# Optimization experiments

Hardware: AMD Instinct MI355X
Metric: run time of the kernel (lower is better)

## Reference

```python
import jax, jax.numpy as jnp
import numpy as np

B, T, D, H, DH, F, E, TOPK = 4, 1024, 1024, 16, 64, 4096, 8, 2
GATE_TEMP = 0.9
EPS = 1e-5


def _ln(x, g, b):
    m = jnp.mean(x, axis=-1, keepdims=True)
    v = jnp.mean((x - m) ** 2, axis=-1, keepdims=True)
    return (x - m) * jax.lax.rsqrt(v + EPS) * g + b


def setup_inputs() -> dict:
    key = jax.random.key(0)
    ks = jax.random.split(key, 16)
    s = 0.02
    inp = {
        'x': jax.random.normal(ks[0], (B, T, D), jnp.float32),
        'mask': jnp.tril(jnp.ones((1, 1, T, T), jnp.int32)),  # causal
        'ln1_g': jnp.ones((D,), jnp.float32), 'ln1_b': jnp.zeros((D,), jnp.float32),
        'wq': jax.random.normal(ks[1], (D, D), jnp.float32) * s, 'bq': jnp.zeros((D,), jnp.float32),
        'wk': jax.random.normal(ks[2], (D, D), jnp.float32) * s, 'bk': jnp.zeros((D,), jnp.float32),
        'wv': jax.random.normal(ks[3], (D, D), jnp.float32) * s, 'bv': jnp.zeros((D,), jnp.float32),
        'wo': jax.random.normal(ks[4], (D, D), jnp.float32) * s, 'bo': jnp.zeros((D,), jnp.float32),
        'ln2_g': jnp.ones((D,), jnp.float32), 'ln2_b': jnp.zeros((D,), jnp.float32),
        'gate_w': jax.random.normal(ks[5], (D, E), jnp.float32) * s, 'gate_b': jnp.zeros((E,), jnp.float32),
        'we1': jax.random.normal(ks[6], (E, D, F), jnp.float32) * s, 'be1': jnp.zeros((E, F), jnp.float32),
        'we2': jax.random.normal(ks[7], (E, F, D), jnp.float32) * s, 'be2': jnp.zeros((E, D), jnp.float32),
        'pn_g': jnp.ones((D,), jnp.float32), 'pn_b': jnp.zeros((D,), jnp.float32),
    }
    return inp


def reference(x, mask, ln1_g, ln1_b, wq, bq, wk, bk, wv, bv, wo, bo,
              ln2_g, ln2_b, gate_w, gate_b, we1, be1, we2, be2, pn_g, pn_b):
    # ---- attention branch (dropout = identity in eval) ----
    h = _ln(x, ln1_g, ln1_b)
    q = (h @ wq + bq).reshape(B, T, H, DH).transpose(0, 2, 1, 3)  # [B,H,T,DH]
    k = (h @ wk + bk).reshape(B, T, H, DH).transpose(0, 2, 1, 3)
    v = (h @ wv + bv).reshape(B, T, H, DH).transpose(0, 2, 1, 3)
    att = jnp.einsum('bhtd,bhsd->bhts', q, k) / jnp.sqrt(jnp.float32(DH))
    att = jnp.where(mask == 0, jnp.float32(-1e9), att)
    att = jax.nn.softmax(att, axis=-1)
    out = jnp.einsum('bhts,bhsd->bhtd', att, v).transpose(0, 2, 1, 3).reshape(B, T, D)
    x = x + (out @ wo + bo)

    # ---- MoE branch ----
    h = _ln(x, ln2_g, ln2_b)
    gate_logits = (h @ gate_w + gate_b) / GATE_TEMP        # [B,T,E]
    topk_vals, topk_idx = jax.lax.top_k(gate_logits, TOPK)
    keep = jnp.sum(jax.nn.one_hot(topk_idx, E, dtype=bool), axis=-2)  # [B,T,E] bool
    masked = jnp.where(keep, gate_logits, -jnp.inf)
    gate_probs = jax.nn.softmax(masked, axis=-1)            # [B,T,E]
    # dense all-expert FFN (exact GELU, dropout=identity)
    hid = jax.nn.gelu(jnp.einsum('btd,edf->btef', h, we1) + be1, approximate=False)
    expert_out = jnp.einsum('btef,efd->bted', hid, we2) + be2  # [B,T,E,D]
    moe = jnp.sum(gate_probs[..., None] * expert_out, axis=2)
    moe = _ln(moe, pn_g, pn_b)
    return x + moe
```

## Files before the change

### kernel.cpp

```cpp
#include <hip/hip_runtime.h>
#include <hip/hip_bf16.h>
#include <math.h>

#define B_ 4
#define T_ 1024
#define D_ 1024
#define H_ 16
#define DH_ 64
#define F_ 4096
#define E_ 8
#define NTOK 4096
#define EPS_ 1e-5f

typedef float f32x4 __attribute__((ext_vector_type(4)));
typedef __bf16 bf16x8 __attribute__((ext_vector_type(8)));
typedef _Float16 f16x8 __attribute__((ext_vector_type(8)));

__device__ __forceinline__ unsigned short f2bf(float f) {
    unsigned u = __float_as_uint(f);
    u = u + 0x7fffu + ((u >> 16) & 1u);
    return (unsigned short)(u >> 16);
}

__device__ __forceinline__ void splitf(float x, unsigned short& h, unsigned short& l) {
    _Float16 hf = (_Float16)x;
    _Float16 lf = (_Float16)((x - (float)hf) * 2048.0f);
    h = __builtin_bit_cast(unsigned short, hf);
    l = __builtin_bit_cast(unsigned short, lf);
}

__device__ __forceinline__ void blockreduce2(float& s, float& sq) {
    #pragma unroll
    for (int o = 32; o > 0; o >>= 1) { s += __shfl_xor(s, o); sq += __shfl_xor(sq, o); }
    __shared__ float ls[4], lq[4];
    int w = threadIdx.x >> 6;
    if ((threadIdx.x & 63) == 0) { ls[w] = s; lq[w] = sq; }
    __syncthreads();
    s = ls[0] + ls[1] + ls[2] + ls[3];
    sq = lq[0] + lq[1] + lq[2] + lq[3];
}

__global__ void k_zero(int* __restrict__ cnt) {
    if (threadIdx.x < E_) cnt[threadIdx.x] = 0;
}

__global__ void k_tconv(const float* __restrict__ in, unsigned short* __restrict__ out,
                        int R, int C) {
    __shared__ float tile[32][33];
    int e = blockIdx.z;
    const float* ine = in + (size_t)e * R * C;
    unsigned short* oute = out + (size_t)e * R * C;
    int tx = threadIdx.x & 31, ty = threadIdx.x >> 5;
    int c0 = blockIdx.x * 32, r0 = blockIdx.y * 32;
    #pragma unroll
    for (int j = 0; j < 32; j += 8)
        tile[ty + j][tx] = ine[(size_t)(r0 + ty + j) * C + c0 + tx];
    __syncthreads();
    #pragma unroll
    for (int j = 0; j < 32; j += 8)
        oute[(size_t)(c0 + ty + j) * R + r0 + tx] = f2bf(tile[tx][ty + j]);
}

__global__ void k_tconv_split(const float* __restrict__ w0, const float* __restrict__ w1,
        const float* __restrict__ w2, const float* __restrict__ w3,
        unsigned short* __restrict__ ohi, unsigned short* __restrict__ olo) {
    __shared__ float tile[32][33];
    int z = blockIdx.z;
    const float* in = (z == 0) ? w0 : ((z == 1) ? w1 : ((z == 2) ? w2 : w3));
    unsigned short* oh = ohi + (size_t)z * D_ * D_;
    unsigned short* ol = olo + (size_t)z * D_ * D_;
    int tx = threadIdx.x & 31, ty = threadIdx.x >> 5;
    int c0 = blockIdx.x * 32, r0 = blockIdx.y * 32;
    #pragma unroll
    for (int j = 0; j < 32; j += 8)
        tile[ty + j][tx] = in[(size_t)(r0 + ty + j) * D_ + c0 + tx];
    __syncthreads();
    #pragma unroll
    for (int j = 0; j < 32; j += 8) {
        unsigned short h, l;
        splitf(tile[tx][ty + j], h, l);
        size_t o = (size_t)(c0 + ty + j) * D_ + r0 + tx;
        oh[o] = h; ol[o] = l;
    }
}

__global__ void k_ln1(const float* __restrict__ x, const float* __restrict__ g,
                      const float* __restrict__ b, unsigned short* __restrict__ hh,
                      unsigned short* __restrict__ hl) {
    int row = blockIdx.x, t = threadIdx.x;
    f32x4 v = *(const f32x4*)(x + (size_t)row * D_ + t * 4);
    float s = v.x + v.y + v.z + v.w;
    float sq = v.x * v.x + v.y * v.y + v.z * v.z + v.w * v.w;
    blockreduce2(s, sq);
    float mean = s * (1.0f / D_);
    float var = sq * (1.0f / D_) - mean * mean;
    float inv = rsqrtf(var + EPS_);
    f32x4 gv = *(const f32x4*)(g + t * 4);
    f32x4 bv = *(const f32x4*)(b + t * 4);
    ushort4 oh, ol;
    float o0 = (v.x - mean) * inv * gv.x + bv.x;
    float o1 = (v.y - mean) * inv * gv.y + bv.y;
    float o2 = (v.z - mean) * inv * gv.z + bv.z;
    float o3 = (v.w - mean) * inv * gv.w + bv.w;
    splitf(o0, oh.x, ol.x); splitf(o1, oh.y, ol.y);
    splitf(o2, oh.z, ol.z); splitf(o3, oh.w, ol.w);
    *(ushort4*)(hh + (size_t)row * D_ + t * 4) = oh;
    *(ushort4*)(hl + (size_t)row * D_ + t * 4) = ol;
}

#define LDK2 40
__device__ __forceinline__ void mfma_split(const unsigned short* __restrict__ Ah,
        const unsigned short* __restrict__ Al, int strideA, int m0,
        const unsigned short* __restrict__ Bh, const unsigned short* __restrict__ Bl,
        int strideB, int n0, int K, f32x4 acc1[4][4], f32x4 acc2[4][4]) {
    __shared__ unsigned short AsH[128 * LDK2];
    __shared__ unsigned short AsL[128 * LDK2];
    __shared__ unsigned short BsH[128 * LDK2];
    __shared__ unsigned short BsL[128 * LDK2];
    int t = threadIdx.x;
    int lane = t & 63, w = t >> 6;
    int wm = (w >> 1) * 64, wn = (w & 1) * 64;
    int r = t >> 1, kc = (t & 1) * 16;
    const unsigned short* pAh = Ah + (size_t)(m0 + r) * strideA + kc;
    const unsigned short* pAl = Al + (size_t)(m0 + r) * strideA + kc;
    const unsigned short* pBh = Bh + (size_t)(n0 + r) * strideB + kc;
    const unsigned short* pBl = Bl + (size_t)(n0 + r) * strideB + kc;
    int c15 = lane & 15, fk = (lane >> 4) * 8;
    unsigned short* wAh = &AsH[r * LDK2 + kc];
    unsigned short* wAl = &AsL[r * LDK2 + kc];
    unsigned short* wBh = &BsH[r * LDK2 + kc];
    unsigned short* wBl = &BsL[r * LDK2 + kc];
    uint4 ah0 = *(const uint4*)(pAh);
    uint4 ah1 = *(const uint4*)(pAh + 8);
    uint4 al0 = *(const uint4*)(pAl);
    uint4 al1 = *(const uint4*)(pAl + 8);
    uint4 bh0 = *(const uint4*)(pBh);
    uint4 bh1 = *(const uint4*)(pBh + 8);
    uint4 bl0 = *(const uint4*)(pBl);
    uint4 bl1 = *(const uint4*)(pBl + 8);
    for (int k0 = 0; k0 < K; k0 += 32) {
        __syncthreads();
        *(uint4*)(wAh) = ah0; *(uint4*)(wAh + 8) = ah1;
        *(uint4*)(wAl) = al0; *(uint4*)(wAl + 8) = al1;
        *(uint4*)(wBh) = bh0; *(uint4*)(wBh + 8) = bh1;
        *(uint4*)(wBl) = bl0; *(uint4*)(wBl + 8) = bl1;
        __syncthreads();
        if (k0 + 32 < K) {
            ah0 = *(const uint4*)(pAh + k0 + 32);
            ah1 = *(const uint4*)(pAh + k0 + 40);
            al0 = *(const uint4*)(pAl + k0 + 32);
            al1 = *(const uint4*)(pAl + k0 + 40);
            bh0 = *(const uint4*)(pBh + k0 + 32);
            bh1 = *(const uint4*)(pBh + k0 + 40);
            bl0 = *(const uint4*)(pBl + k0 + 32);
            bl1 = *(const uint4*)(pBl + k0 + 40);
        }
        f16x8 bfh[4], bfl[4];
        #pragma unroll
        for (int i = 0; i < 4; i++) {
            bfh[i] = *(const f16x8*)(&BsH[(wn + c15 + i * 16) * LDK2 + fk]);
            bfl[i] = *(const f16x8*)(&BsL[(wn + c15 + i * 16) * LDK2 + fk]);
        }
        #pragma unroll
        for (int mi = 0; mi < 4; mi++) {
            f16x8 afh = *(const f16x8*)(&AsH[(wm + c15 + mi * 16) * LDK2 + fk]);
            f16x8 afl = *(const f16x8*)(&AsL[(wm + c15 + mi * 16) * LDK2 + fk]);
            #pragma unroll
            for (int ni = 0; ni < 4; ni++) {
                acc1[mi][ni] = __builtin_amdgcn_mfma_f32_16x16x32_f16(afh, bfh[ni], acc1[mi][ni], 0, 0, 0);
                acc2[mi][ni] = __builtin_amdgcn_mfma_f32_16x16x32_f16(afh, bfl[ni], acc2[mi][ni], 0, 0, 0);
                acc2[mi][ni] = __builtin_amdgcn_mfma_f32_16x16x32_f16(afl, bfh[ni], acc2[mi][ni], 0, 0, 0);
            }
        }
    }
}

__global__ __launch_bounds__(256, 2) void k_qkv_split(
        const unsigned short* __restrict__ h1h, const unsigned short* __restrict__ h1l,
        const unsigned short* __restrict__ wth, const unsigned short* __restrict__ wtl,
        const float* __restrict__ bq, const float* __restrict__ bk, const float* __restrict__ bv,
        unsigned short* __restrict__ Qh, unsigned short* __restrict__ Ql,
        unsigned short* __restrict__ Kh, unsigned short* __restrict__ Kl,
        unsigned short* __restrict__ Vh, unsigned short* __restrict__ Vl) {
    int which = blockIdx.z;
    const unsigned short* Bh = wth + (size_t)which * D_ * D_;
    const unsigned short* Bl = wtl + (size_t)which * D_ * D_;
    const float* bias = (which == 0) ? bq : ((which == 1) ? bk : bv);
    unsigned short* Oh = (which == 0) ? Qh : ((which == 1) ? Kh : Vh);
    unsigned short* Ol = (which == 0) ? Ql : ((which == 1) ? Kl : Vl);
    f32x4 a1[4][4], a2[4][4];
    #pragma unroll
    for (int i = 0; i < 4; i++)
        #pragma unroll
        for (int j = 0; j < 4; j++) {
            a1[i][j].x = 0.f; a1[i][j].y = 0.f; a1[i][j].z = 0.f; a1[i][j].w = 0.f;
            a2[i][j].x = 0.f; a2[i][j].y = 0.f; a2[i][j].z = 0.f; a2[i][j].w = 0.f;
        }
    int m0 = blockIdx.y * 128, n0 = blockIdx.x * 128;
    mfma_split(h1h, h1l, D_, m0, Bh, Bl, D_, n0, D_, a1, a2);
    int lane = threadIdx.x & 63, w = threadIdx.x >> 6;
    int wm = (w >> 1) * 64, wn = (w & 1) * 64;
    int c15 = lane & 15, quad = lane >> 4;
    #pragma unroll
    for (int mi = 0; mi < 4; mi++) {
        #pragma unroll
        for (int rr = 0; rr < 4; rr++) {
            int row = m0 + wm + mi * 16 + quad * 4 + rr;
            int bidx = row >> 10, tt = row & 1023;
            #pragma unroll
            for (int ni = 0; ni < 4; ni++) {
                int col = n0 + wn + ni * 16 + c15;
                float vv = a1[mi][ni][rr] + a2[mi][ni][rr] * (1.0f / 2048.0f) + bias[col];
                unsigned short hs, ls;
                splitf(vv, hs, ls);
                size_t idx = (((size_t)bidx * H_ + (col >> 6)) * T_ + tt) * DH_ + (col & 63);
                Oh[idx] = hs; Ol[idx] = ls;
            }
        }
    }
}

__global__ __launch_bounds__(256, 2) void k_proj_split(
        const unsigned short* __restrict__ ah, const unsigned short* __restrict__ al,
        const unsigned short* __restrict__ wh, const unsigned short* __restrict__ wl,
        float* __restrict__ xp) {
    int ks = blockIdx.z;
    f32x4 a1[4][4], a2[4][4];
    #pragma unroll
    for (int i = 0; i < 4; i++)
        #pragma unroll
        for (int j = 0; j < 4; j++) {
            a1[i][j].x = 0.f; a1[i][j].y = 0.f; a1[i][j].z = 0.f; a1[i][j].w = 0.f;
            a2[i][j].x = 0.f; a2[i][j].y = 0.f; a2[i][j].z = 0.f; a2[i][j].w = 0.f;
        }
    int m0 = blockIdx.y * 128, n0 = blockIdx.x * 128;
    mfma_split(ah + ks * 512, al + ks * 512, D_, m0,
               wh + ks * 512, wl + ks * 512, D_, n0, 512, a1, a2);
    float* dst = xp + (size_t)ks * NTOK * D_;
    int lane = threadIdx.x & 63, w = threadIdx.x >> 6;
    int wm = (w >> 1) * 64, wn = (w & 1) * 64;
    int c15 = lane & 15, quad = lane >> 4;
    #pragma unroll
    for (int mi = 0; mi < 4; mi++) {
        #pragma unroll
        for (int rr = 0; rr < 4; rr++) {
            int row = m0 + wm + mi * 16 + quad * 4 + rr;
            #pragma unroll
            for (int ni = 0; ni < 4; ni++) {
                int col = n0 + wn + ni * 16 + c15;
                dst[(size_t)row * D_ + col] = a1[mi][ni][rr] + a2[mi][ni][rr] * (1.0f / 2048.0f);
            }
        }
    }
}

#define NSLOT 40
__device__ __forceinline__ int slot_base(int qt) {
    const int base[16] = {0,1,2,3,4,6,8,10,12,15,18,21,24,28,32,36};
    return base[qt];
}
__device__ __forceinline__ int swzb(int r, int cb) {
    return r * 128 + (cb ^ ((r & 7) << 4));
}
__global__ __launch_bounds__(256, 2) void k_attn1(
        const unsigned short* __restrict__ Qh, const unsigned short* __restrict__ Ql,
        const unsigned short* __restrict__ Kh, const unsigned short* __restrict__ Kl,
        const unsigned short* __restrict__ Vh, const unsigned short* __restrict__ Vl,
        float* __restrict__ opart, float* __restrict__ mlpart) {
    __shared__ unsigned short QsH[64 * 64], QsL[64 * 64];
    __shared__ unsigned short KsH[64 * 64], KsL[64 * 64];
    __shared__ unsigned short VtH[64 * 64], VtL[64 * 64];
    __shared__ unsigned short PsH[64 * 64], PsL[64 * 64];
    int sp = blockIdx.x, qt = blockIdx.y, bh = blockIdx.z;
    int lim = (qt + 1) * 64;
    int s0 = sp * 256;
    if (s0 >= lim) return;
    int ntile = min(4, (lim - s0) >> 6);
    int t = threadIdx.x;
    int lane = t & 63, w = t >> 6;
    int c15 = lane & 15, quad = lane >> 4;
    size_t bho = (size_t)bh * T_ * DH_;
    {
        int q = t >> 2, cb = (t & 3) * 32;
        const unsigned short* sh = Qh + bho + (size_t)(qt * 64 + q) * DH_ + (cb >> 1);
        const unsigned short* sl = Ql + bho + (size_t)(qt * 64 + q) * DH_ + (cb >> 1);
        uint4 h0 = *(const uint4*)(sh);
        uint4 h1 = *(const uint4*)(sh + 8);
        uint4 l0 = *(const uint4*)(sl);
        uint4 l1 = *(const uint4*)(sl + 8);
        *(uint4*)((char*)QsH + swzb(q, cb))      = h0;
        *(uint4*)((char*)QsH + swzb(q, cb + 16)) = h1;
        *(uint4*)((char*)QsL + swzb(q, cb))      = l0;
        *(uint4*)((char*)QsL + swzb(q, cb + 16)) = l1;
    }
    f32x4 o1[4], o2[4];
    #pragma unroll
    for (int i = 0; i < 4; i++) {
        o1[i].x = 0.f; o1[i].y = 0.f; o1[i].z = 0.f; o1[i].w = 0.f;
        o2[i].x = 0.f; o2[i].y = 0.f; o2[i].z = 0.f; o2[i].w = 0.f;
    }
    float m[4] = {-1e30f, -1e30f, -1e30f, -1e30f};
    float l[4] = {0.f, 0.f, 0.f, 0.f};
    int qglob0 = qt * 64 + w * 16 + quad * 4;
    for (int kt = 0; kt < ntile; kt++) {
        int kbase = s0 + kt * 64;
        __syncthreads();
        {
            int r = t >> 2, cb = (t & 3) * 32;
            const unsigned short* sh = Kh + bho + (size_t)(kbase + r) * DH_ + (cb >> 1);
            const unsigned short* sl = Kl + bho + (size_t)(kbase + r) * DH_ + (cb >> 1);
            uint4 h0 = *(const uint4*)(sh);
            uint4 h1 = *(const uint4*)(sh + 8);
            uint4 l0 = *(const uint4*)(sl);
            uint4 l1 = *(const uint4*)(sl + 8);
            *(uint4*)((char*)KsH + swzb(r, cb))      = h0;
            *(uint4*)((char*)KsH + swzb(r, cb + 16)) = h1;
            *(uint4*)((char*)KsL + swzb(r, cb))      = l0;
            *(uint4*)((char*)KsL + swzb(r, cb + 16)) = l1;
        }
        {
            int k = t & 63, d0 = (t >> 6) * 16;
            const unsigned short* vh = Vh + bho + (size_t)(kbase + k) * DH_ + d0;
            const unsigned short* vl = Vl + bho + (size_t)(kbase + k) * DH_ + d0;
            unsigned short hv[16], lv[16];
            *(uint4*)(hv) = *(const uint4*)(vh);
            *(uint4*)(hv + 8) = *(const uint4*)(vh + 8);
            *(uint4*)(lv) = *(const uint4*)(vl);
            *(uint4*)(lv + 8) = *(const uint4*)(vl + 8);
            #pragma unroll
            for (int i = 0; i < 16; i++) {
                int d = d0 + i;
                *(unsigned short*)((char*)VtH + swzb(d, k * 2)) = hv[i];
                *(unsigned short*)((char*)VtL + swzb(d, k * 2)) = lv[i];
            }
        }
        __syncthreads();
        f32x4 s1[4], s2[4];
        #pragma unroll
        for (int i = 0; i < 4; i++) {
            s1[i].x = 0.f; s1[i].y = 0.f; s1[i].z = 0.f; s1[i].w = 0.f;
            s2[i].x = 0.f; s2[i].y = 0.f; s2[i].z = 0.f; s2[i].w = 0.f;
        }
        #pragma unroll
        for (int kk = 0; kk < 2; kk++) {
            int cb = kk * 64 + quad * 16;
            f16x8 ah = *(const f16x8*)((char*)QsH + swzb(w * 16 + c15, cb));
            f16x8 al = *(const f16x8*)((char*)QsL + swzb(w * 16 + c15, cb));
            #pragma unroll
            for (int ni = 0; ni < 4; ni++) {
                f16x8 bh16 = *(const f16x8*)((char*)KsH + swzb(ni * 16 + c15, cb));
                f16x8 bl16 = *(const f16x8*)((char*)KsL + swzb(ni * 16 + c15, cb));
                s1[ni] = __builtin_amdgcn_mfma_f32_16x16x32_f16(ah, bh16, s1[ni], 0, 0, 0);
                s2[ni] = __builtin_amdgcn_mfma_f32_16x16x32_f16(ah, bl16, s2[ni], 0, 0, 0);
                s2[ni] = __builtin_amdgcn_mfma_f32_16x16x32_f16(al, bh16, s2[ni], 0, 0, 0);
            }
        }
        f32x4 p[4];
        #pragma unroll
        for (int ni = 0; ni < 4; ni++)
            p[ni] = s1[ni] * 0.125f + s2[ni] * 6.103515625e-5f;
        #pragma unroll
        for (int ni = 0; ni < 4; ni++) {
            int kglob = kbase + c15 + 16 * ni;
            #pragma unroll
            for (int r = 0; r < 4; r++)
                p[ni][r] = (kglob <= qglob0 + r) ? p[ni][r] : -1e30f;
        }
        float alpha[4];
        #pragma unroll
        for (int r = 0; r < 4; r++) {
            float rm = fmaxf(fmaxf(p[0][r], p[1][r]), fmaxf(p[2][r], p[3][r]));
            rm = fmaxf(rm, __shfl_xor(rm, 1));
            rm = fmaxf(rm, __shfl_xor(rm, 2));
            rm = fmaxf(rm, __shfl_xor(rm, 4));
            rm = fmaxf(rm, __shfl_xor(rm, 8));
            float mnew = fmaxf(m[r], rm);
            alpha[r] = __expf(m[r] - mnew);
            m[r] = mnew;
            float rs = 0.f;
            #pragma unroll
            for (int ni = 0; ni < 4; ni++) {
                float pv = (p[ni][r] > -1e29f) ? __expf(p[ni][r] - mnew) : 0.f;
                p[ni][r] = pv;
                rs += pv;
            }
            rs += __shfl_xor(rs, 1);
            rs += __shfl_xor(rs, 2);
            rs += __shfl_xor(rs, 4);
            rs += __shfl_xor(rs, 8);
            l[r] = l[r] * alpha[r] + rs;
        }
        #pragma unroll
        for (int ni = 0; ni < 4; ni++) {
            o1[ni].x *= alpha[0]; o1[ni].y *= alpha[1]; o1[ni].z *= alpha[2]; o1[ni].w *= alpha[3];
            o2[ni].x *= alpha[0]; o2[ni].y *= alpha[1]; o2[ni].z *= alpha[2]; o2[ni].w *= alpha[3];
        }
        #pragma unroll
        for (int ni = 0; ni < 4; ni++) {
            int cbyte = (c15 + 16 * ni) * 2;
            #pragma unroll
            for (int r = 0; r < 4; r++) {
                unsigned short hs, ls;
                splitf(p[ni][r], hs, ls);
                int row = w * 16 + quad * 4 + r;
                *(unsigned short*)((char*)PsH + swzb(row, cbyte)) = hs;
                *(unsigned short*)((char*)PsL + swzb(row, cbyte)) = ls;
            }
        }
        __syncthreads();
        #pragma unroll
        for (int kk = 0; kk < 2; kk++) {
            int cb = kk * 64 + quad * 16;
            f16x8 ph = *(const f16x8*)((char*)PsH + swzb(w * 16 + c15, cb));
            f16x8 pl = *(const f16x8*)((char*)PsL + swzb(w * 16 + c15, cb));
            #pragma unroll
            for (int ni = 0; ni < 4; ni++) {
                f16x8 vh16 = *(const f16x8*)((char*)VtH + swzb(ni * 16 + c15, cb));
                f16x8 vl16 = *(const f16x8*)((char*)VtL + swzb(ni * 16 + c15, cb));
                o1[ni] = __builtin_amdgcn_mfma_f32_16x16x32_f16(ph, vh16, o1[ni], 0, 0, 0);
                o2[ni] = __builtin_amdgcn_mfma_f32_16x16x32_f16(ph, vl16, o2[ni], 0, 0, 0);
                o2[ni] = __builtin_amdgcn_mfma_f32_16x16x32_f16(pl, vh16, o2[ni], 0, 0, 0);
            }
        }
    }
    int slot = bh * NSLOT + slot_base(qt) + sp;
    float* dst = opart + (size_t)slot * 64 * 64;
    #pragma unroll
    for (int ni = 0; ni < 4; ni++) {
        #pragma unroll
        for (int r = 0; r < 4; r++) {
            float val = o1[ni][r] + o2[ni][r] * (1.0f / 2048.0f);
            dst[(size_t)(w * 16 + quad * 4 + r) * 64 + c15 + 16 * ni] = val;
        }
    }
    if (c15 == 0) {
        #pragma unroll
        for (int r = 0; r < 4; r++) {
            int row = w * 16 + quad * 4 + r;
            mlpart[slot * 128 + row * 2 + 0] = m[r];
            mlpart[slot * 128 + row * 2 + 1] = l[r];
        }
    }
}

__global__ void k_attn2(const float* __restrict__ opart, const float* __restrict__ mlpart,
                        unsigned short* __restrict__ atth, unsigned short* __restrict__ attl) {
    int qt = blockIdx.x, bh = blockIdx.y;
    int b = bh >> 4, h = bh & 15;
    int nsp = (qt >> 2) + 1;
    int slot0 = bh * NSLOT + slot_base(qt);
    int tid = threadIdx.x;
    int q = tid >> 2, d0 = (tid & 3) * 16;
    float ms[4], ls[4];
    float mx = -1e30f;
    for (int s = 0; s < nsp; s++) {
        ms[s] = mlpart[(slot0 + s) * 128 + q * 2 + 0];
        ls[s] = mlpart[(slot0 + s) * 128 + q * 2 + 1];
        mx = fmaxf(mx, ms[s]);
    }
    float den = 0.f;
    f32x4 num[4];
    #pragma unroll
    for (int i = 0; i < 4; i++) { num[i].x = 0.f; num[i].y = 0.f; num[i].z = 0.f; num[i].w = 0.f; }
    for (int s = 0; s < nsp; s++) {
        float sc = __expf(ms[s] - mx);
        den += ls[s] * sc;
        const float* src = opart + ((size_t)(slot0 + s) * 64 + q) * 64 + d0;
        #pragma unroll
        for (int i = 0; i < 4; i++) num[i] += sc * *(const f32x4*)(src + i * 4);
    }
    float inv = 1.0f / den;
    size_t base = ((size_t)(b * T_ + qt * 64 + q)) * D_ + h * DH_ + d0;
    #pragma unroll
    for (int i = 0; i < 4; i++) {
        f32x4 v = num[i] * inv;
        ushort4 hh, ll;
        splitf(v.x, hh.x, ll.x); splitf(v.y, hh.y, ll.y);
        splitf(v.z, hh.z, ll.z); splitf(v.w, hh.w, ll.w);
        *(ushort4*)(atth + base + i * 4) = hh;
        *(ushort4*)(attl + base + i * 4) = ll;
    }
}

__global__ void k_ln2_gate(const float* __restrict__ xp, const float* __restrict__ bo,
        const float* __restrict__ xin, float* __restrict__ x2,
        const float* __restrict__ g, const float* __restrict__ bb,
        const float* __restrict__ gw, const float* __restrict__ gb,
        unsigned short* __restrict__ h2, int* __restrict__ cnt, int* __restrict__ lst,
        int* __restrict__ te, int* __restrict__ ts, float* __restrict__ tp) {
    int row = blockIdx.x, t = threadIdx.x;
    f32x4 v = *(const f32x4*)(xp + (size_t)row * D_ + t * 4)
            + *(const f32x4*)(xp + (size_t)NTOK * D_ + (size_t)row * D_ + t * 4)
            + *(const f32x4*)(bo + t * 4)
            + *(const f32x4*)(xin + (size_t)row * D_ + t * 4);
    *(f32x4*)(x2 + (size_t)row * D_ + t * 4) = v;
    float s = v.x + v.y + v.z + v.w;
    float sq = v.x * v.x + v.y * v.y + v.z * v.z + v.w * v.w;
    blockreduce2(s, sq);
    float mean = s * (1.0f / D_), var = sq * (1.0f / D_) - mean * mean;
    float inv = rsqrtf(var + EPS_);
    f32x4 gv = *(const f32x4*)(g + t * 4);
    f32x4 bv = *(const f32x4*)(bb + t * 4);
    float hv[4];
    #pragma unroll
    for (int i = 0; i < 4; i++) hv[i] = (v[i] - mean) * inv * gv[i] + bv[i];
    ushort4 hb;
    hb.x = f2bf(hv[0]); hb.y = f2bf(hv[1]); hb.z = f2bf(hv[2]); hb.w = f2bf(hv[3]);
    *(ushort4*)(&h2[(size_t)row * D_ + t * 4]) = hb;
    float lg[8];
    #pragma unroll
    for (int e2 = 0; e2 < 8; e2++) lg[e2] = 0.f;
    #pragma unroll
    for (int i = 0; i < 4; i++) {
        const float* gr = gw + (size_t)(t * 4 + i) * E_;
        f32x4 g0 = *(const f32x4*)(gr);
        f32x4 g1 = *(const f32x4*)(gr + 4);
        lg[0] = fmaf(hv[i], g0.x, lg[0]); lg[1] = fmaf(hv[i], g0.y, lg[1]);
        lg[2] = fmaf(hv[i], g0.z, lg[2]); lg[3] = fmaf(hv[i], g0.w, lg[3]);
        lg[4] = fmaf(hv[i], g1.x, lg[4]); lg[5] = fmaf(hv[i], g1.y, lg[5]);
        lg[6] = fmaf(hv[i], g1.z, lg[6]); lg[7] = fmaf(hv[i], g1.w, lg[7]);
    }
    #pragma unroll
    for (int o = 32; o > 0; o >>= 1) {
        #pragma unroll
        for (int e2 = 0; e2 < 8; e2++) lg[e2] += __shfl_xor(lg[e2], o);
    }
    __shared__ float lred[4][8];
    int w = t >> 6;
    if ((t & 63) == 0) {
        #pragma unroll
        for (int e2 = 0; e2 < 8; e2++) lred[w][e2] = lg[e2];
    }
    __syncthreads();
    if (t == 0) {
        float L[8];
        #pragma unroll
        for (int e2 = 0; e2 < 8; e2++)
            L[e2] = (lred[0][e2] + lred[1][e2] + lred[2][e2] + lred[3][e2] + gb[e2]) / 0.9f;
        int e0 = 0, e1 = -1; float v0 = L[0], v1 = -3e38f;
        #pragma unroll
        for (int e2 = 1; e2 < 8; e2++) {
            float xv = L[e2];
            if (xv > v0)      { v1 = v0; e1 = e0; v0 = xv; e0 = e2; }
            else if (xv > v1) { v1 = xv; e1 = e2; }
        }
        float ex = __expf(v1 - v0);
        float denom = 1.0f + ex;
        float p0 = 1.0f / denom, p1 = ex / denom;
        int s0 = atomicAdd(&cnt[e0], 1);
        int s1 = atomicAdd(&cnt[e1], 1);
        lst[e0 * NTOK + s0] = row;
        lst[e1 * NTOK + s1] = row;
        te[row * 2 + 0] = e0; te[row * 2 + 1] = e1;
        ts[row * 2 + 0] = s0; ts[row * 2 + 1] = s1;
        tp[row * 2 + 0] = p0; tp[row * 2 + 1] = p1;
    }
}

__global__ void k_offs(const int* __restrict__ cnt, int* __restrict__ offs) {
    if (threadIdx.x == 0 && blockIdx.x == 0) {
        int a = 0;
        #pragma unroll
        for (int e = 0; e < E_; e++) { offs[e] = a; a += cnt[e]; }
    }
}

#define LDK 40
__device__ __forceinline__ void mfma_core(const unsigned short* __restrict__ A, int strideA,
        const int* __restrict__ gather, int m0, int M,
        const unsigned short* __restrict__ Bt, int strideB, int n0, int K, f32x4 acc[4][4]) {
    __shared__ unsigned short As[128 * LDK];
    __shared__ unsigned short Bs[128 * LDK];
    int t = threadIdx.x;
    int lane = t & 63, w = t >> 6;
    int wm = (w >> 1) * 64, wn = (w & 1) * 64;
    int r = t >> 1, kc = (t & 1) * 16;
    int arow;
    if (gather) { int mm = m0 + r; arow = gather[mm < M ? mm : 0]; }
    else arow = m0 + r;
    const unsigned short* Ap = A + (size_t)arow * strideA + kc;
    const unsigned short* Bp = Bt + (size_t)(n0 + r) * strideB + kc;
    int c15 = lane & 15, fk = (lane >> 4) * 8;
    unsigned short* AsW = &As[r * LDK + kc];
    unsigned short* BsW = &Bs[r * LDK + kc];
    uint4 a0 = *(const uint4*)(Ap);
    uint4 a1 = *(const uint4*)(Ap + 8);
    uint4 b0 = *(const uint4*)(Bp);
    uint4 b1 = *(const uint4*)(Bp + 8);
    for (int k0 = 0; k0 < K; k0 += 32) {
        __syncthreads();
        *(uint4*)(AsW) = a0; *(uint4*)(AsW + 8) = a1;
        *(uint4*)(BsW) = b0; *(uint4*)(BsW + 8) = b1;
        __syncthreads();
        if (k0 + 32 < K) {
            a0 = *(const uint4*)(Ap + k0 + 32);
            a1 = *(const uint4*)(Ap + k0 + 40);
            b0 = *(const uint4*)(Bp + k0 + 32);
            b1 = *(const uint4*)(Bp + k0 + 40);
        }
        bf16x8 af[4], bfr[4];
        #pragma unroll
        for (int i = 0; i < 4; i++) {
            af[i]  = *(const bf16x8*)(&As[(wm + c15 + i * 16) * LDK + fk]);
            bfr[i] = *(const bf16x8*)(&Bs[(wn + c15 + i * 16) * LDK + fk]);
        }
        #pragma unroll
        for (int mi = 0; mi < 4; mi++)
            #pragma unroll
            for (int ni = 0; ni < 4; ni++)
                acc[mi][ni] = __builtin_amdgcn_mfma_f32_16x16x32_bf16(af[mi], bfr[ni], acc[mi][ni], 0, 0, 0);
    }
}

__global__ __launch_bounds__(256, 2) void k_moe1(const unsigned short* __restrict__ h2,
        const unsigned short* __restrict__ w1t, const float* __restrict__ be1,
        const int* __restrict__ cnt, const int* __restrict__ offs, const int* __restrict__ lst,
        unsigned short* __restrict__ hid) {
    int e = blockIdx.z;
    int M = cnt[e];
    int m0 = blockIdx.y * 128;
    if (m0 >= M) return;
    int n0 = blockIdx.x * 128;
    f32x4 acc[4][4];
    #pragma unroll
    for (int i = 0; i < 4; i++)
        #pragma unroll
        for (int j = 0; j < 4; j++) { acc[i][j].x = 0.f; acc[i][j].y = 0.f; acc[i][j].z = 0.f; acc[i][j].w = 0.f; }
    mfma_core(h2, D_, lst + e * NTOK, m0, M, w1t + (size_t)e * F_ * D_, D_, n0, D_, acc);
    int lane = threadIdx.x & 63, w = threadIdx.x >> 6;
    int wm = (w >> 1) * 64, wn = (w & 1) * 64;
    int base = offs[e];
    const float* b1 = be1 + (size_t)e * F_;
    int c15 = lane & 15, quad = lane >> 4;
    #pragma unroll
    for (int mi = 0; mi < 4; mi++) {
        #pragma unroll
        for (int rr = 0; rr < 4; rr++) {
            int row = m0 + wm + mi * 16 + quad * 4 + rr;
            if (row < M) {
                size_t rb = (size_t)(base + row) * F_;
                #pragma unroll
                for (int ni = 0; ni < 4; ni++) {
                    int col = n0 + wn + ni * 16 + c15;
                    float xv = acc[mi][ni][rr] + b1[col];
                    float ge = 0.5f * xv * (1.0f + erff(xv * 0.70710678118654752f));
                    hid[rb + col] = f2bf(ge);
                }
            }
        }
    }
}

__global__ __launch_bounds__(256, 2) void k_moe2(const unsigned short* __restrict__ hid,
        const unsigned short* __restrict__ w2t,
        const int* __restrict__ cnt, const int* __restrict__ offs, float* __restrict__ eop) {
    int ez = blockIdx.z;
    int e = ez >> 1, ks = ez & 1;
    int M = cnt[e];
    int m0 = blockIdx.y * 128;
    if (m0 >= M) return;
    int n0 = blockIdx.x * 128;
    int base = offs[e];
    f32x4 acc[4][4];
    #pragma unroll
    for (int i = 0; i < 4; i++)
        #pragma unroll
        for (int j = 0; j < 4; j++) { acc[i][j].x = 0.f; acc[i][j].y = 0.f; acc[i][j].z = 0.f; acc[i][j].w = 0.f; }
    mfma_core(hid + (size_t)base * F_ + ks * (F_ / 2), F_, nullptr, m0, M,
              w2t + (size_t)e * D_ * F_ + ks * (F_ / 2), F_, n0, F_ / 2, acc);
    float* dst = eop + (size_t)ks * 2 * NTOK * D_ + (size_t)base * D_;
    int lane = threadIdx.x & 63, w = threadIdx.x >> 6;
    int wm = (w >> 1) * 64, wn = (w & 1) * 64;
    int c15 = lane & 15, quad = lane >> 4;
    #pragma unroll
    for (int mi = 0; mi < 4; mi++) {
        #pragma unroll
        for (int rr = 0; rr < 4; rr++) {
            int row = m0 + wm + mi * 16 + quad * 4 + rr;
            if (row < M) {
                #pragma unroll
                for (int ni = 0; ni < 4; ni++) {
                    int col = n0 + wn + ni * 16 + c15;
                    dst[(size_t)row * D_ + col] = acc[mi][ni][rr];
                }
            }
        }
    }
}

__global__ void k_final(const float* __restrict__ x2, const float* __restrict__ eop,
        const float* __restrict__ be2,
        const int* __restrict__ te, const int* __restrict__ ts, const float* __restrict__ tp,
        const int* __restrict__ offs, const float* __restrict__ png, const float* __restrict__ pnb,
        float* __restrict__ out) {
    int row = blockIdx.x, t = threadIdx.x;
    int e0 = te[row * 2], e1 = te[row * 2 + 1];
    size_t g0 = (size_t)(offs[e0] + ts[row * 2]);
    size_t g1 = (size_t)(offs[e1] + ts[row * 2 + 1]);
    float p0 = tp[row * 2], p1 = tp[row * 2 + 1];
    const size_t HALF = (size_t)2 * NTOK * D_;
    f32x4 a = *(const f32x4*)(eop + g0 * D_ + t * 4)
            + *(const f32x4*)(eop + HALF + g0 * D_ + t * 4)
            + *(const f32x4*)(be2 + (size_t)e0 * D_ + t * 4);
    f32x4 b = *(const f32x4*)(eop + g1 * D_ + t * 4)
            + *(const f32x4*)(eop + HALF + g1 * D_ + t * 4)
            + *(const f32x4*)(be2 + (size_t)e1 * D_ + t * 4);
    f32x4 mo = p0 * a + p1 * b;
    float s = mo.x + mo.y + mo.z + mo.w;
    float sq = mo.x * mo.x + mo.y * mo.y + mo.z * mo.z + mo.w * mo.w;
    blockreduce2(s, sq);
    float mean = s * (1.0f / D_), var = sq * (1.0f / D_) - mean * mean;
    float inv = rsqrtf(var + EPS_);
    f32x4 gv = *(const f32x4*)(png + t * 4);
    f32x4 bv = *(const f32x4*)(pnb + t * 4);
    f32x4 xv = *(const f32x4*)(x2 + (size_t)row * D_ + t * 4);
    f32x4 o;
    o.x = xv.x + (mo.x - mean) * inv * gv.x + bv.x;
    o.y = xv.y + (mo.y - mean) * inv * gv.y + bv.y;
    o.z = xv.z + (mo.z - mean) * inv * gv.z + bv.z;
    o.w = xv.w + (mo.w - mean) * inv * gv.w + bv.w;
    *(f32x4*)(out + (size_t)row * D_ + t * 4) = o;
}

extern "C" void kernel_launch(void* const* d_in, const int* in_sizes, int n_in,
                              void* d_out, int out_size, void* d_ws, size_t ws_size,
                              hipStream_t stream) {
    (void)in_sizes; (void)n_in; (void)out_size; (void)ws_size;
    const float* x    = (const float*)d_in[0];
    const float* ln1g = (const float*)d_in[2];
    const float* ln1b = (const float*)d_in[3];
    const float* wq   = (const float*)d_in[4];
    const float* bq   = (const float*)d_in[5];
    const float* wk   = (const float*)d_in[6];
    const float* bk   = (const float*)d_in[7];
    const float* wv   = (const float*)d_in[8];
    const float* bv   = (const float*)d_in[9];
    const float* wo   = (const float*)d_in[10];
    const float* bo   = (const float*)d_in[11];
    const float* ln2g = (const float*)d_in[12];
    const float* ln2b = (const float*)d_in[13];
    const float* gw   = (const float*)d_in[14];
    const float* gb   = (const float*)d_in[15];
    const float* we1  = (const float*)d_in[16];
    const float* be1  = (const float*)d_in[17];
    const float* we2  = (const float*)d_in[18];
    const float* be2  = (const float*)d_in[19];
    const float* png  = (const float*)d_in[20];
    const float* pnb  = (const float*)d_in[21];
    float* out = (float*)d_out;

    char* ws = (char*)d_ws;
    size_t off = 0;
    auto alloc = [&](size_t bytes) { void* p = ws + off; off += (bytes + 255) & ~(size_t)255; return p; };
    unsigned short* h1h = (unsigned short*)alloc((size_t)NTOK * D_ * 2);
    unsigned short* h1l = (unsigned short*)alloc((size_t)NTOK * D_ * 2);
    unsigned short* Qhp = (unsigned short*)alloc((size_t)NTOK * D_ * 2);
    unsigned short* Qlp = (unsigned short*)alloc((size_t)NTOK * D_ * 2);
    unsigned short* Khp = (unsigned short*)alloc((size_t)NTOK * D_ * 2);
    unsigned short* Klp = (unsigned short*)alloc((size_t)NTOK * D_ * 2);
    unsigned short* Vhp = (unsigned short*)alloc((size_t)NTOK * D_ * 2);
    unsigned short* Vlp = (unsigned short*)alloc((size_t)NTOK * D_ * 2);
    unsigned short* atth = (unsigned short*)alloc((size_t)NTOK * D_ * 2);
    unsigned short* attl = (unsigned short*)alloc((size_t)NTOK * D_ * 2);
    float* x2  = (float*)alloc((size_t)NTOK * D_ * 4);
    unsigned short* h2  = (unsigned short*)alloc((size_t)NTOK * D_ * 2);
    unsigned short* w1t = (unsigned short*)alloc((size_t)E_ * D_ * F_ * 2);
    unsigned short* w2t = (unsigned short*)alloc((size_t)E_ * D_ * F_ * 2);
    unsigned short* hid = (unsigned short*)alloc((size_t)(2 * NTOK + 128) * F_ * 2);
    float* opart = (float*)alloc((size_t)64 * NSLOT * 64 * 64 * 4);
    float* mlpart= (float*)alloc((size_t)64 * NSLOT * 128 * 4);
    unsigned short* wsh = (unsigned short*)alloc((size_t)4 * D_ * D_ * 2);
    unsigned short* wsl = (unsigned short*)alloc((size_t)4 * D_ * D_ * 2);
    int* cnt   = (int*)alloc(256);
    int* offs  = (int*)alloc(256);
    int* lst   = (int*)alloc((size_t)E_ * NTOK * 4);
    int* te    = (int*)alloc((size_t)NTOK * 2 * 4);
    int* ts    = (int*)alloc((size_t)NTOK * 2 * 4);
    float* tp  = (float*)alloc((size_t)NTOK * 2 * 4);
    float* xp  = opart;
    float* eop = (float*)h1h;

    k_zero<<<dim3(1), dim3(64), 0, stream>>>(cnt);
    k_tconv<<<dim3(F_ / 32, D_ / 32, E_), dim3(256), 0, stream>>>(we1, w1t, D_, F_);
    k_tconv<<<dim3(D_ / 32, F_ / 32, E_), dim3(256), 0, stream>>>(we2, w2t, F_, D_);
    k_tconv_split<<<dim3(D_ / 32, D_ / 32, 4), dim3(256), 0, stream>>>(wq, wk, wv, wo, wsh, wsl);
    k_ln1<<<dim3(NTOK), dim3(256), 0, stream>>>(x, ln1g, ln1b, h1h, h1l);
    k_qkv_split<<<dim3(D_ / 128, NTOK / 128, 3), dim3(256), 0, stream>>>(
        h1h, h1l, wsh, wsl, bq, bk, bv, Qhp, Qlp, Khp, Klp, Vhp, Vlp);
    k_attn1<<<dim3(4, T_ / 64, B_ * H_), dim3(256), 0, stream>>>(
        Qhp, Qlp, Khp, Klp, Vhp, Vlp, opart, mlpart);
    k_attn2<<<dim3(T_ / 64, B_ * H_), dim3(256), 0, stream>>>(opart, mlpart, atth, attl);
    k_proj_split<<<dim3(D_ / 128, NTOK / 128, 2), dim3(256), 0, stream>>>(
        atth, attl, wsh + (size_t)3 * D_ * D_, wsl + (size_t)3 * D_ * D_, xp);
    k_ln2_gate<<<dim3(NTOK), dim3(256), 0, stream>>>(
        xp, bo, x, x2, ln2g, ln2b, gw, gb, h2, cnt, lst, te, ts, tp);
    k_offs<<<dim3(1), dim3(64), 0, stream>>>(cnt, offs);
    k_moe1<<<dim3(F_ / 128, NTOK / 128, E_), dim3(256), 0, stream>>>(h2, w1t, be1, cnt, offs, lst, hid);
    k_moe2<<<dim3(D_ / 128, NTOK / 128, E_ * 2), dim3(256), 0, stream>>>(hid, w2t, cnt, offs, eop);
    k_final<<<dim3(NTOK), dim3(256), 0, stream>>>(x2, eop, be2, te, ts, tp, offs, png, pnb, out);
}
```

Measured before the change: 1.022 ms.

## Use direct global-to-LDS loads, XCD block swizzle, and fast erf in MoE GEMMs

Replaces the register-staged global-to-shared copy in the MoE GEMM core with global_load_lds direct transfers into an unpadded 32-wide LDS tile. This drops the register prefetch of the next k-slice, so loads are no longer overlapped with the MFMA work. Block indices in both MoE kernels are remapped so that consecutive blocks spread across XCDs, aiming for better L2 locality. The exact erff in the GELU epilogue is replaced by an Abramowitz-Stegun polynomial approximation, which has a small accuracy error (about 1e-7 absolute on erf).

After: 968.1 us. 1.06x faster.

```diff
diff --git a/kernel.cpp b/kernel.cpp
--- a/kernel.cpp
+++ b/kernel.cpp
@@ -27,6 +27,22 @@
     _Float16 lf = (_Float16)((x - (float)hf) * 2048.0f);
     h = __builtin_bit_cast(unsigned short, hf);
     l = __builtin_bit_cast(unsigned short, lf);
+}
+
+__device__ __forceinline__ float erf_fast(float x) {
+    float ax = fabsf(x);
+    float t = 1.0f / fmaf(0.3275911f, ax, 1.0f);
+    float y = t * fmaf(t, fmaf(t, fmaf(t, fmaf(t, 1.061405429f, -1.453152027f),
+                  1.421413741f), -0.284496736f), 0.254829592f);
+    float r = 1.0f - y * __expf(-ax * ax);
+    return copysignf(r, x);
+}
+
+__device__ __forceinline__ void gload16(const unsigned short* g, unsigned short* l) {
+    __builtin_amdgcn_global_load_lds(
+        (const __attribute__((address_space(1))) unsigned int*)g,
+        (__attribute__((address_space(3))) unsigned int*)l,
+        16, 0, 0);
 }
 
 __device__ __forceinline__ void blockreduce2(float& s, float& sq) {
@@ -565,44 +581,43 @@
     }
 }
 
-#define LDK 40
 __device__ __forceinline__ void mfma_core(const unsigned short* __restrict__ A, int strideA,
         const int* __restrict__ gather, int m0, int M,
         const unsigned short* __restrict__ Bt, int strideB, int n0, int K, f32x4 acc[4][4]) {
-    __shared__ unsigned short As[128 * LDK];
-    __shared__ unsigned short Bs[128 * LDK];
+    __shared__ unsigned short As[128 * 32];
+    __shared__ unsigned short Bs[128 * 32];
     int t = threadIdx.x;
-    int lane = t & 63, w = t >> 6;
-    int wm = (w >> 1) * 64, wn = (w & 1) * 64;
-    int r = t >> 1, kc = (t & 1) * 16;
-    int arow;
-    if (gather) { int mm = m0 + r; arow = gather[mm < M ? mm : 0]; }
-    else arow = m0 + r;
-    const unsigned short* Ap = A + (size_t)arow * strideA + kc;
-    const unsigned short* Bp = Bt + (size_t)(n0 + r) * strideB + kc;
+    int lane = t & 63, wid = t >> 6;
+    int wm = (wid >> 1) * 64, wn = (wid & 1) * 64;
     int c15 = lane & 15, fk = (lane >> 4) * 8;
-    unsigned short* AsW = &As[r * LDK + kc];
-    unsigned short* BsW = &Bs[r * LDK + kc];
-    uint4 a0 = *(const uint4*)(Ap);
-    uint4 a1 = *(const uint4*)(Ap + 8);
-    uint4 b0 = *(const uint4*)(Bp);
-    uint4 b1 = *(const uint4*)(Bp + 8);
+    int r0 = wid * 32 + (lane >> 2);
+    int kc2 = (lane & 3) * 8;
+    int ar0, ar1;
+    {
+        int mm0 = m0 + r0, mm1 = m0 + r0 + 16;
+        if (gather) { ar0 = gather[mm0 < M ? mm0 : 0]; ar1 = gather[mm1 < M ? mm1 : 0]; }
+        else        { ar0 = mm0; ar1 = mm1; }
+    }
+    const unsigned short* pA0 = A + (size_t)ar0 * strideA + kc2;
+    const unsigned short* pA1 = A + (size_t)ar1 * strideA + kc2;
+    const unsigned short* pB0 = Bt + (size_t)(n0 + r0) * strideB + kc2;
+    const unsigned short* pB1 = Bt + (size_t)(n0 + r0 + 16) * strideB + kc2;
+    unsigned short* lA0 = As + (wid * 2 + 0) * 512;
+    unsigned short* lA1 = As + (wid * 2 + 1) * 512;
+    unsigned short* lB0 = Bs + (wid * 2 + 0) * 512;
+    unsigned short* lB1 = Bs + (wid * 2 + 1) * 512;
     for (int k0 = 0; k0 < K; k0 += 32) {
         __syncthreads();
-        *(uint4*)(AsW) = a0; *(uint4*)(AsW + 8) = a1;
-        *(uint4*)(BsW) = b0; *(uint4*)(BsW + 8) = b1;
+        gload16(pA0 + k0, lA0);
+        gload16(pA1 + k0, lA1);
+        gload16(pB0 + k0, lB0);
+        gload16(pB1 + k0, lB1);
         __syncthreads();
-        if (k0 + 32 < K) {
-            a0 = *(const uint4*)(Ap + k0 + 32);
-            a1 = *(const uint4*)(Ap + k0 + 40);
-            b0 = *(const uint4*)(Bp + k0 + 32);
-            b1 = *(const uint4*)(Bp + k0 + 40);
-        }
         bf16x8 af[4], bfr[4];
         #pragma unroll
         for (int i = 0; i < 4; i++) {
-            af[i]  = *(const bf16x8*)(&As[(wm + c15 + i * 16) * LDK + fk]);
-            bfr[i] = *(const bf16x8*)(&Bs[(wn + c15 + i * 16) * LDK + fk]);
+            af[i]  = *(const bf16x8*)(&As[(wm + c15 + i * 16) * 32 + fk]);
+            bfr[i] = *(const bf16x8*)(&Bs[(wn + c15 + i * 16) * 32 + fk]);
         }
         #pragma unroll
         for (int mi = 0; mi < 4; mi++)
@@ -616,11 +631,13 @@
         const unsigned short* __restrict__ w1t, const float* __restrict__ be1,
         const int* __restrict__ cnt, const int* __restrict__ offs, const int* __restrict__ lst,
         unsigned short* __restrict__ hid) {
-    int e = blockIdx.z;
+    int flat = blockIdx.x + (blockIdx.y << 5) + (blockIdx.z << 10);
+    int sfl = ((flat & 7) << 10) + (flat >> 3);
+    int bx = sfl & 31, by = (sfl >> 5) & 31, e = sfl >> 10;
     int M = cnt[e];
-    int m0 = blockIdx.y * 128;
+    int m0 = by * 128;
     if (m0 >= M) return;
-    int n0 = blockIdx.x * 128;
+    int n0 = bx * 128;
     f32x4 acc[4][4];
     #pragma unroll
     for (int i = 0; i < 4; i++)
@@ -643,7 +660,7 @@
                 for (int ni = 0; ni < 4; ni++) {
                     int col = n0 + wn + ni * 16 + c15;
                     float xv = acc[mi][ni][rr] + b1[col];
-                    float ge = 0.5f * xv * (1.0f + erff(xv * 0.70710678118654752f));
+                    float ge = 0.5f * xv * (1.0f + erf_fast(xv * 0.70710678118654752f));
                     hid[rb + col] = f2bf(ge);
                 }
             }
@@ -654,12 +671,14 @@
 __global__ __launch_bounds__(256, 2) void k_moe2(const unsigned short* __restrict__ hid,
         const unsigned short* __restrict__ w2t,
         const int* __restrict__ cnt, const int* __restrict__ offs, float* __restrict__ eop) {
-    int ez = blockIdx.z;
+    int flat = blockIdx.x + (blockIdx.y << 3) + (blockIdx.z << 8);
+    int sfl = ((flat & 7) << 9) + (flat >> 3);
+    int bx = sfl & 7, by = (sfl >> 3) & 31, ez = sfl >> 8;
     int e = ez >> 1, ks = ez & 1;
     int M = cnt[e];
-    int m0 = blockIdx.y * 128;
+    int m0 = by * 128;
     if (m0 >= M) return;
-    int n0 = blockIdx.x * 128;
+    int n0 = bx * 128;
     int base = offs[e];
     f32x4 acc[4][4];
     #pragma unroll
```
